# Optimization experiments

Measured on AMD Instinct MI355X. Metric: run time of the kernel, lower is better.

## Reference

```python
import jax, jax.numpy as jnp
import numpy as np

HEADS = 16

def _split_qkv(qkv, h):
    # faithful to rearrange 'b t (d k h) -> k b h t d' with k=3
    b, t, e3 = qkv.shape
    d = e3 // (3 * h)
    qkv = qkv.reshape(b, t, d, 3, h)          # (b,t,d,k,h), d-major packing
    qkv = jnp.transpose(qkv, (3, 0, 4, 1, 2))  # (k,b,h,t,d)
    return qkv[0], qkv[1], qkv[2]

def setup_inputs() -> dict:
    key = jax.random.key(0)
    ks = jax.random.split(key, 5)
    b, t, e = 2, 2048, 1024
    s = e ** -0.5
    return {
        "x": jax.random.normal(ks[0], (b, t, e), jnp.float32),
        "tx": jax.random.normal(ks[1], (b, t, e), jnp.float32),
        "Wqkv": jax.random.normal(ks[2], (3 * e, e), jnp.float32) * s,
        "Wtqkv": jax.random.normal(ks[3], (3 * e, e), jnp.float32) * s,
        "Wout": jax.random.normal(ks[4], (e, e), jnp.float32) * s,
    }

def reference(x, tx, Wqkv, Wtqkv, Wout):
    h = HEADS
    e = x.shape[-1]
    d_head = e // h
    scale = jnp.float32(d_head ** 0.5)  # NOTE: module MULTIPLIES by sqrt(d_head)

    qkv = x @ Wqkv.T     # (b,t,3e)
    tqkv = tx @ Wtqkv.T  # (b,t,3e)
    _q, k, v = _split_qkv(qkv, h)      # each (b,h,t,d)
    tq, _tk, _tv = _split_qkv(tqkv, h)

    energy = jnp.einsum('bhid,bhjd->bhij', tq, k) * scale  # (b,h,t,t)
    attn = jax.nn.softmax(energy, axis=-1)
    out = jnp.einsum('bhij,bhjd->bhid', attn, v)           # (b,h,t,d)
    b, _, t, d = out.shape
    out = jnp.transpose(out, (0, 2, 1, 3)).reshape(b, t, h * d)  # 'b h t d -> b t (h d)'
    return out @ Wout.T
```

## Files before the change

### kernel.cpp

```cpp
#include <hip/hip_runtime.h>

typedef unsigned short u16;
typedef unsigned int u32;
typedef __attribute__((ext_vector_type(8))) short short8;
typedef __attribute__((ext_vector_type(4))) float f32x4;

__device__ inline u16 f32_to_bf16(float f) {
  u32 u = __float_as_uint(f);
  u += 0x7fffu + ((u >> 16) & 1u);
  return (u16)(u >> 16);
}
__device__ inline float bf16_to_f32(u16 s) {
  return __uint_as_float(((u32)s) << 16);
}

#if __has_builtin(__builtin_amdgcn_exp2f)
#define EXP2F(x) __builtin_amdgcn_exp2f(x)
#else
#define EXP2F(x) exp2f(x)
#endif

__device__ inline void dma16(const void* gp, void* lp) {
  __builtin_amdgcn_global_load_lds(
      (const __attribute__((address_space(1))) u32*)gp,
      (__attribute__((address_space(3))) u32*)lp, 16, 0, 0);
}

__device__ inline u32 pack_hi16(u32 a, u32 b) {
  return __builtin_amdgcn_perm(b, a, 0x07060302u);
}
__device__ inline uint4 pack_bf16_8(const uint4 a, const uint4 b) {
  uint4 r;
  r.x = pack_hi16(a.x, a.y);
  r.y = pack_hi16(a.z, a.w);
  r.z = pack_hi16(b.x, b.y);
  r.w = pack_hi16(b.z, b.w);
  return r;
}
__device__ inline void split8(const uint4 a, const uint4 b, uint4& hi, uint4& lo) {
  u32 u[8] = {a.x, a.y, a.z, a.w, b.x, b.y, b.z, b.w};
  u32 l[8];
#pragma unroll
  for (int j = 0; j < 8; ++j)
    l[j] = __float_as_uint(__uint_as_float(u[j]) - __uint_as_float(u[j] & 0xffff0000u));
  hi.x = pack_hi16(u[0], u[1]); hi.y = pack_hi16(u[2], u[3]);
  hi.z = pack_hi16(u[4], u[5]); hi.w = pack_hi16(u[6], u[7]);
  lo.x = pack_hi16(l[0], l[1]); lo.y = pack_hi16(l[2], l[3]);
  lo.z = pack_hi16(l[4], l[5]); lo.w = pack_hi16(l[6], l[7]);
}

__global__ void repack_w(const float* __restrict__ Wqkv, const float* __restrict__ Wtqkv,
                         const float* __restrict__ Wout,
                         u16* __restrict__ Wtq_hi, u16* __restrict__ Wtq_lo,
                         u16* __restrict__ Wk_hi,  u16* __restrict__ Wk_lo,
                         u16* __restrict__ Wv_hi,  u16* __restrict__ Woutb) {
  int r = blockIdx.x;
  int part = r >> 10;
  int rr = r & 1023;
  int h = rr >> 6, d = rr & 63;
  const float* src;
  u16 *dh, *dl = nullptr;
  if (part == 0)      { src = Wtqkv + (size_t)(d * 48 + h) * 1024;      dh = Wtq_hi + (size_t)rr * 1024; dl = Wtq_lo + (size_t)rr * 1024; }
  else if (part == 1) { src = Wqkv  + (size_t)(d * 48 + 16 + h) * 1024; dh = Wk_hi  + (size_t)rr * 1024; dl = Wk_lo  + (size_t)rr * 1024; }
  else if (part == 2) { src = Wqkv  + (size_t)(d * 48 + 32 + h) * 1024; dh = Wv_hi  + (size_t)rr * 1024; }
  else                { src = Wout  + (size_t)rr * 1024;                dh = Woutb  + (size_t)rr * 1024; }
  int c = threadIdx.x * 4;
  f32x4 v = *(const f32x4*)&src[c];
  u32 hv[4], lv[4];
#pragma unroll
  for (int j = 0; j < 4; ++j) {
    u16 hb = f32_to_bf16(v[j]);
    hv[j] = hb;
    lv[j] = f32_to_bf16(v[j] - bf16_to_f32(hb));
  }
  uint2 ho; ho.x = hv[0] | (hv[1] << 16); ho.y = hv[2] | (hv[3] << 16);
  *(uint2*)&dh[c] = ho;
  if (dl) {
    uint2 lo; lo.x = lv[0] | (lv[1] << 16); lo.y = lv[2] | (lv[3] << 16);
    *(uint2*)&dl[c] = lo;
  }
}

__global__ __launch_bounds__(256) __attribute__((amdgpu_waves_per_eu(2)))
void proj_fused(const float* __restrict__ x, const float* __restrict__ tx,
                const u16* __restrict__ Wtq_hi, const u16* __restrict__ Wtq_lo,
                const u16* __restrict__ Wk_hi,  const u16* __restrict__ Wk_lo,
                const u16* __restrict__ Wv_hi,
                u16* __restrict__ Qhi, u16* __restrict__ Qlo,
                u16* __restrict__ Khi, u16* __restrict__ Klo,
                u16* __restrict__ Vt, float qscale) {
  __shared__ __align__(16) float Fs[2][128][32];
  __shared__ __align__(16) u16   Hs[2][128][32];
  __shared__ __align__(16) u16   Ls[2][128][32];
  const int tid = threadIdx.x;
  const int wid = tid >> 6, lane = tid & 63;
  const int g = lane >> 4, l16 = lane & 15;
  const int job = blockIdx.y;
  const int tile = blockIdx.x;
  const int wm = (wid & 1) * 64, wn = (wid >> 1) * 64;

  int m0, n0, N, frow0, hrow0;
  const float* Fsrc;
  const u16 *Hsrc;
  const u16 *Lsrc = nullptr;
  if (job == 0) {
    m0 = (tile >> 3) * 128; n0 = (tile & 7) * 128; N = 1024;
    Fsrc = tx; frow0 = m0; Hsrc = Wtq_hi; Lsrc = Wtq_lo; hrow0 = n0;
  } else if (job == 1) {
    m0 = (tile >> 3) * 128; n0 = (tile & 7) * 128; N = 1024;
    Fsrc = x; frow0 = m0; Hsrc = Wk_hi; Lsrc = Wk_lo; hrow0 = n0;
  } else {
    m0 = (tile >> 5) * 128; n0 = (tile & 31) * 128; N = 4096;
    Fsrc = x; frow0 = n0; Hsrc = Wv_hi; hrow0 = m0;
  }

  const int lrow8 = lane >> 3;
  const int gf = (lane & 7) ^ lrow8;
  const int lrow4 = lane >> 2;
  const int gh = (lane & 3) ^ ((lrow4 ^ (lrow4 >> 2)) & 3);

  auto issue_chunk = [&](int k0, int p) {
#pragma unroll
    for (int t = 0; t < 4; ++t) {
      int rb = wid * 32 + t * 8;
      dma16(&Fsrc[(size_t)(frow0 + rb + lrow8) * 1024 + k0 + gf * 4], &Fs[p][rb][0]);
    }
#pragma unroll
    for (int t = 0; t < 2; ++t) {
      int rb = wid * 32 + t * 16;
      size_t ro = (size_t)(hrow0 + rb + lrow4) * 1024 + k0 + gh * 8;
      dma16(&Hsrc[ro], &Hs[p][rb][0]);
      if (job != 2) dma16(&Lsrc[ro], &Ls[p][rb][0]);
    }
  };

  f32x4 acc[4][4];
  const f32x4 zero4 = {0.f, 0.f, 0.f, 0.f};
#pragma unroll
  for (int i = 0; i < 4; ++i)
#pragma unroll
    for (int j = 0; j < 4; ++j) acc[i][j] = zero4;

  const int sw8 = l16 & 7;
  const int sw4 = (l16 ^ (l16 >> 2)) & 3;

  issue_chunk(0, 0);

  for (int k0 = 0; k0 < 1024; k0 += 32) {
    const int p = (k0 >> 5) & 1;
    __syncthreads();
    if (k0 + 32 < 1024) issue_chunk(k0 + 32, p ^ 1);

    if (job != 2) {
      short8 ah[4], al[4], bh4[4], bl4[4];
#pragma unroll
      for (int mi = 0; mi < 4; ++mi) {
        const int R = wm + mi * 16 + l16;
        uint4 u0 = *(const uint4*)&Fs[p][R][((2 * g) ^ sw8) * 4];
        uint4 u1 = *(const uint4*)&Fs[p][R][((2 * g + 1) ^ sw8) * 4];
        uint4 hi, lo;
        split8(u0, u1, hi, lo);
        ah[mi] = *(short8*)&hi;
        al[mi] = *(short8*)&lo;
      }
#pragma unroll
      for (int ni = 0; ni < 4; ++ni) {
        const int R = wn + ni * 16 + l16;
        const int col = (g ^ sw4) * 8;
        bh4[ni] = *(const short8*)&Hs[p][R][col];
        bl4[ni] = *(const short8*)&Ls[p][R][col];
      }
#pragma unroll
      for (int mi = 0; mi < 4; ++mi)
#pragma unroll
        for (int ni = 0; ni < 4; ++ni) {
          acc[mi][ni] = __builtin_amdgcn_mfma_f32_16x16x32_bf16(ah[mi], bh4[ni], acc[mi][ni], 0, 0, 0);
          acc[mi][ni] = __builtin_amdgcn_mfma_f32_16x16x32_bf16(ah[mi], bl4[ni], acc[mi][ni], 0, 0, 0);
          acc[mi][ni] = __builtin_amdgcn_mfma_f32_16x16x32_bf16(al[mi], bh4[ni], acc[mi][ni], 0, 0, 0);
        }
    } else {
      short8 av[4], bx[4];
#pragma unroll
      for (int mi = 0; mi < 4; ++mi)
        av[mi] = *(const short8*)&Hs[p][wm + mi * 16 + l16][(g ^ sw4) * 8];
#pragma unroll
      for (int ni = 0; ni < 4; ++ni) {
        const int R = wn + ni * 16 + l16;
        uint4 u0 = *(const uint4*)&Fs[p][R][((2 * g) ^ sw8) * 4];
        uint4 u1 = *(const uint4*)&Fs[p][R][((2 * g + 1) ^ sw8) * 4];
        uint4 t = pack_bf16_8(u0, u1);
        bx[ni] = *(short8*)&t;
      }
#pragma unroll
      for (int mi = 0; mi < 4; ++mi)
#pragma unroll
        for (int ni = 0; ni < 4; ++ni)
          acc[mi][ni] = __builtin_amdgcn_mfma_f32_16x16x32_bf16(av[mi], bx[ni], acc[mi][ni], 0, 0, 0);
    }
  }

  u16* Chi = (job == 0) ? Qhi : ((job == 1) ? Khi : Vt);
  u16* Clo = (job == 0) ? Qlo : Klo;
  float scale = (job == 0) ? qscale : 1.0f;
#pragma unroll
  for (int mi = 0; mi < 4; ++mi)
#pragma unroll
    for (int ni = 0; ni < 4; ++ni) {
      int row = m0 + wm + mi * 16 + g * 4;
      int col = n0 + wn + ni * 16 + l16;
#pragma unroll
      for (int r = 0; r < 4; ++r) {
        float v = acc[mi][ni][r] * scale;
        size_t o = (size_t)(row + r) * N + col;
        u32 uv = __float_as_uint(v);
        if (job != 2) {
          Chi[o] = (u16)(uv >> 16);
          float lo = v - __uint_as_float(uv & 0xffff0000u);
          Clo[o] = (u16)(__float_as_uint(lo) >> 16);
        } else {
          Chi[o] = (u16)(uv >> 16);
        }
      }
    }
}

__global__ __launch_bounds__(256) __attribute__((amdgpu_waves_per_eu(2, 4)))
void gemm_out(const u16* __restrict__ A, const u16* __restrict__ B,
              float* __restrict__ C, int M, int N, int K) {
  __shared__ __align__(16) u16 As[128][40];
  __shared__ __align__(16) u16 Bs[64][40];
  const int tid = threadIdx.x;
  const int wid = tid >> 6, lane = tid & 63;
  const int g = lane >> 4, l16 = lane & 15;
  const int m0 = blockIdx.y * 128, n0 = blockIdx.x * 64;
  const int wm = (wid & 1) * 64, wn = (wid >> 1) * 32;

  f32x4 acc[4][2];
  const f32x4 zero4 = {0.f, 0.f, 0.f, 0.f};
#pragma unroll
  for (int i = 0; i < 4; ++i)
#pragma unroll
    for (int j = 0; j < 2; ++j) acc[i][j] = zero4;

  uint4 pa[2], pb;
  const int rowA0 = tid >> 2, colA = (tid & 3) * 8;
  const int rowA1 = rowA0 + 64;
  const int rowB = tid >> 2, colB = (tid & 3) * 8;
  pa[0] = *(const uint4*)&A[(size_t)(m0 + rowA0) * K + colA];
  pa[1] = *(const uint4*)&A[(size_t)(m0 + rowA1) * K + colA];
  pb    = *(const uint4*)&B[(size_t)(n0 + rowB) * K + colB];

  for (int k0 = 0; k0 < K; k0 += 32) {
    __syncthreads();
    *(uint4*)&As[rowA0][colA] = pa[0];
    *(uint4*)&As[rowA1][colA] = pa[1];
    *(uint4*)&Bs[rowB][colB] = pb;
    __syncthreads();
    if (k0 + 32 < K) {
      pa[0] = *(const uint4*)&A[(size_t)(m0 + rowA0) * K + k0 + 32 + colA];
      pa[1] = *(const uint4*)&A[(size_t)(m0 + rowA1) * K + k0 + 32 + colA];
      pb    = *(const uint4*)&B[(size_t)(n0 + rowB) * K + k0 + 32 + colB];
    }
    short8 af[4], bfr[2];
#pragma unroll
    for (int mi = 0; mi < 4; ++mi)
      af[mi] = *(const short8*)&As[wm + mi * 16 + l16][g * 8];
#pragma unroll
    for (int ni = 0; ni < 2; ++ni)
      bfr[ni] = *(const short8*)&Bs[wn + ni * 16 + l16][g * 8];
#pragma unroll
    for (int mi = 0; mi < 4; ++mi)
#pragma unroll
      for (int ni = 0; ni < 2; ++ni)
        acc[mi][ni] = __builtin_amdgcn_mfma_f32_16x16x32_bf16(af[mi], bfr[ni], acc[mi][ni], 0, 0, 0);
  }
#pragma unroll
  for (int mi = 0; mi < 4; ++mi)
#pragma unroll
    for (int ni = 0; ni < 2; ++ni) {
      int row = m0 + wm + mi * 16 + g * 4;
      int col = n0 + wn + ni * 16 + l16;
#pragma unroll
      for (int r = 0; r < 4; ++r)
        C[(size_t)(row + r) * N + col] = acc[mi][ni][r];
    }
}

__global__ __launch_bounds__(256)
void attn_fwd(const u16* __restrict__ Qhi, const u16* __restrict__ Qlo,
              const u16* __restrict__ Khi, const u16* __restrict__ Klo,
              const u16* __restrict__ Vt, u16* __restrict__ O) {
  const int blk = blockIdx.x;
  const int qb = blk & 15, bh = blk >> 4;
  const int h = bh & 15, b = bh >> 4;
  const int t0 = qb * 128;
  const int tid = threadIdx.x, wid = tid >> 6, lane = tid & 63;
  const int g = lane >> 4, l16 = lane & 15;

  __shared__ __align__(16) u16 Ksh[2][64][64];
  __shared__ __align__(16) u16 Ksl[2][64][64];
  __shared__ __align__(16) u16 Vs[2][64][64];
  __shared__ __align__(16) u16 Ps[4][32][72];

  const int lrow = lane >> 3;
  const int lgc  = (lane & 7) ^ lrow;
  const size_t kbase = (size_t)(b * 2048) * 1024 + h * 64;
  const size_t vbase = (size_t)(h * 64) * 4096 + b * 2048;

  auto issue_chunk = [&](int j0, int p) {
#pragma unroll
    for (int t = 0; t < 2; ++t) {
      int rbase = wid * 16 + t * 8;
      int row = rbase + lrow;
      dma16(&Khi[kbase + (size_t)(j0 + row) * 1024 + lgc * 8], &Ksh[p][rbase][0]);
      dma16(&Klo[kbase + (size_t)(j0 + row) * 1024 + lgc * 8], &Ksl[p][rbase][0]);
      dma16(&Vt[vbase + (size_t)row * 4096 + j0 + lgc * 8],    &Vs[p][rbase][0]);
    }
  };

  short8 qh[2][2], ql[2][2];
#pragma unroll
  for (int mt = 0; mt < 2; ++mt)
#pragma unroll
    for (int ks = 0; ks < 2; ++ks) {
      size_t qo = (size_t)(b * 2048 + t0 + wid * 32 + mt * 16 + l16) * 1024
                  + h * 64 + ks * 32 + g * 8;
      qh[mt][ks] = *(const short8*)&Qhi[qo];
      ql[mt][ks] = *(const short8*)&Qlo[qo];
    }

  float mrow[2][4];
#pragma unroll
  for (int mt = 0; mt < 2; ++mt)
#pragma unroll
    for (int r = 0; r < 4; ++r) mrow[mt][r] = -1.0e30f;
  const f32x4 zero4 = {0.f, 0.f, 0.f, 0.f};
  f32x4 acc[2][5];
#pragma unroll
  for (int mt = 0; mt < 2; ++mt)
#pragma unroll
    for (int dn = 0; dn < 5; ++dn) acc[mt][dn] = zero4;

  short8 ones8;
#pragma unroll
  for (int j = 0; j < 8; ++j) ones8[j] = (short)0x3f80;

  issue_chunk(0, 0);

  for (int i = 0; i < 32; ++i) {
    const int p = i & 1;
    __syncthreads();
    if (i < 31) issue_chunk((i + 1) * 64, 1 - p);

    f32x4 s[2][4];
#pragma unroll
    for (int mt = 0; mt < 2; ++mt)
#pragma unroll
      for (int n = 0; n < 4; ++n) s[mt][n] = zero4;
#pragma unroll
    for (int ks = 0; ks < 2; ++ks)
#pragma unroll
      for (int n = 0; n < 4; ++n) {
        int col = (((ks * 4 + g) ^ (l16 & 7))) * 8;
        short8 kh = *(const short8*)&Ksh[p][n * 16 + l16][col];
        short8 kl = *(const short8*)&Ksl[p][n * 16 + l16][col];
        s[0][n] = __builtin_amdgcn_mfma_f32_16x16x32_bf16(qh[0][ks], kh, s[0][n], 0, 0, 0);
        s[1][n] = __builtin_amdgcn_mfma_f32_16x16x32_bf16(qh[1][ks], kh, s[1][n], 0, 0, 0);
        s[0][n] = __builtin_amdgcn_mfma_f32_16x16x32_bf16(ql[0][ks], kh, s[0][n], 0, 0, 0);
        s[1][n] = __builtin_amdgcn_mfma_f32_16x16x32_bf16(ql[1][ks], kh, s[1][n], 0, 0, 0);
        s[0][n] = __builtin_amdgcn_mfma_f32_16x16x32_bf16(qh[0][ks], kl, s[0][n], 0, 0, 0);
        s[1][n] = __builtin_amdgcn_mfma_f32_16x16x32_bf16(qh[1][ks], kl, s[1][n], 0, 0, 0);
      }

#pragma unroll
    for (int mt = 0; mt < 2; ++mt)
#pragma unroll
      for (int r = 0; r < 4; ++r) {
        float cm = fmaxf(fmaxf(s[mt][0][r], s[mt][1][r]),
                         fmaxf(s[mt][2][r], s[mt][3][r]));
        cm = fmaxf(cm, __shfl_xor(cm, 1));
        cm = fmaxf(cm, __shfl_xor(cm, 2));
        cm = fmaxf(cm, __shfl_xor(cm, 4));
        cm = fmaxf(cm, __shfl_xor(cm, 8));
        float mnew = fmaxf(mrow[mt][r], cm);
        float al = EXP2F(mrow[mt][r] - mnew);
        mrow[mt][r] = mnew;
#pragma unroll
        for (int dn = 0; dn < 5; ++dn) acc[mt][dn][r] *= al;
        int qr = mt * 16 + g * 4 + r;
#pragma unroll
        for (int n = 0; n < 4; ++n) {
          float pv = EXP2F(s[mt][n][r] - mnew);
          Ps[wid][qr][n * 16 + l16] = (u16)(__float_as_uint(pv) >> 16);
        }
      }

#pragma unroll
    for (int ks2 = 0; ks2 < 2; ++ks2) {
      short8 pa0 = *(const short8*)&Ps[wid][l16][ks2 * 32 + g * 8];
      short8 pa1 = *(const short8*)&Ps[wid][16 + l16][ks2 * 32 + g * 8];
#pragma unroll
      for (int dn = 0; dn < 4; ++dn) {
        int col = (((ks2 * 4 + g) ^ (l16 & 7))) * 8;
        short8 vb = *(const short8*)&Vs[p][dn * 16 + l16][col];
        acc[0][dn] = __builtin_amdgcn_mfma_f32_16x16x32_bf16(pa0, vb, acc[0][dn], 0, 0, 0);
        acc[1][dn] = __builtin_amdgcn_mfma_f32_16x16x32_bf16(pa1, vb, acc[1][dn], 0, 0, 0);
      }
      acc[0][4] = __builtin_amdgcn_mfma_f32_16x16x32_bf16(pa0, ones8, acc[0][4], 0, 0, 0);
      acc[1][4] = __builtin_amdgcn_mfma_f32_16x16x32_bf16(pa1, ones8, acc[1][4], 0, 0, 0);
    }
  }

#pragma unroll
  for (int mt = 0; mt < 2; ++mt)
#pragma unroll
    for (int r = 0; r < 4; ++r) {
      float inv = 1.f / acc[mt][4][r];
      int row = t0 + wid * 32 + mt * 16 + g * 4 + r;
      size_t base = (size_t)(b * 2048 + row) * 1024 + h * 64;
#pragma unroll
      for (int dn = 0; dn < 4; ++dn)
        O[base + dn * 16 + l16] = (u16)(__float_as_uint(acc[mt][dn][r] * inv) >> 16);
    }
}

extern "C" void kernel_launch(void* const* d_in, const int* in_sizes, int n_in,
                              void* d_out, int out_size, void* d_ws, size_t ws_size,
                              hipStream_t stream) {
  const float* x     = (const float*)d_in[0];
  const float* tx    = (const float*)d_in[1];
  const float* Wqkv  = (const float*)d_in[2];
  const float* Wtqkv = (const float*)d_in[3];
  const float* Wout  = (const float*)d_in[4];
  float* out = (float*)d_out;

  char* ws = (char*)d_ws;
  const size_t MB = 1048576;
  u16* Wtq_hi = (u16*)(ws + 0 * MB);
  u16* Wtq_lo = (u16*)(ws + 2 * MB);
  u16* Wk_hi  = (u16*)(ws + 4 * MB);
  u16* Wk_lo  = (u16*)(ws + 6 * MB);
  u16* Wv_hi  = (u16*)(ws + 8 * MB);
  u16* Woutb  = (u16*)(ws + 10 * MB);
  u16* Qhi    = (u16*)(ws + 12 * MB);
  u16* Qlo    = (u16*)(ws + 20 * MB);
  u16* Khi    = (u16*)(ws + 28 * MB);
  u16* Klo    = (u16*)(ws + 36 * MB);
  u16* Vt     = (u16*)(ws + 44 * MB);
  u16* Ob     = (u16*)(ws + 0 * MB);
  if (ws_size < 52 * MB) return;

  const float QSCALE = 8.0f * 1.4426950408889634f;

  repack_w<<<4096, 256, 0, stream>>>(Wqkv, Wtqkv, Wout,
                                     Wtq_hi, Wtq_lo, Wk_hi, Wk_lo, Wv_hi, Woutb);
  proj_fused<<<dim3(256, 3), 256, 0, stream>>>(x, tx, Wtq_hi, Wtq_lo, Wk_hi, Wk_lo,
                                               Wv_hi, Qhi, Qlo, Khi, Klo, Vt, QSCALE);
  attn_fwd<<<512, 256, 0, stream>>>(Qhi, Qlo, Khi, Klo, Vt, Ob);
  gemm_out<<<dim3(16, 32), 256, 0, stream>>>(Ob, Woutb, out, 4096, 1024, 1024);
}
```

Baseline: 348.0 us.

## Transpose attention MFMAs to keep P in registers instead of LDS

Swaps the MFMA operand order so S and O are computed transposed, which puts each query row in a lane's column. The softmax max then reduces over the lane's own registers plus two cross-lane shuffles instead of four shuffles per element. P is packed to bf16 and redistributed with shuffles rather than round-tripping through the per-wave LDS buffer. The output is written with vectorized 8-byte stores. This removes LDS traffic and shared memory but adds shuffle and select work, and it relies on a pack_hi16 helper that must exist elsewhere in the file.

```diff
diff --git a/kernel.cpp b/kernel.cpp
--- a/kernel.cpp
+++ b/kernel.cpp
@@ -296,11 +296,12 @@
   const int t0 = qb * 128;
   const int tid = threadIdx.x, wid = tid >> 6, lane = tid & 63;
   const int g = lane >> 4, l16 = lane & 15;
+  const int par = g & 1;
+  const int hi2 = g >> 1;
 
   __shared__ __align__(16) u16 Ksh[2][64][64];
   __shared__ __align__(16) u16 Ksl[2][64][64];
   __shared__ __align__(16) u16 Vs[2][64][64];
-  __shared__ __align__(16) u16 Ps[4][32][72];
 
   const int lrow = lane >> 3;
   const int lgc  = (lane & 7) ^ lrow;
@@ -329,11 +330,7 @@
       ql[mt][ks] = *(const short8*)&Qlo[qo];
     }
 
-  float mrow[2][4];
-#pragma unroll
-  for (int mt = 0; mt < 2; ++mt)
-#pragma unroll
-    for (int r = 0; r < 4; ++r) mrow[mt][r] = -1.0e30f;
+  float mrow[2] = {-1.0e30f, -1.0e30f};
   const f32x4 zero4 = {0.f, 0.f, 0.f, 0.f};
   f32x4 acc[2][5];
 #pragma unroll
@@ -344,6 +341,8 @@
   short8 ones8;
 #pragma unroll
   for (int j = 0; j < 8; ++j) ones8[j] = (short)0x3f80;
+
+  union PB { u32 w[4]; short8 v; };
 
   issue_chunk(0, 0);
 
@@ -364,64 +363,82 @@
         int col = (((ks * 4 + g) ^ (l16 & 7))) * 8;
         short8 kh = *(const short8*)&Ksh[p][n * 16 + l16][col];
         short8 kl = *(const short8*)&Ksl[p][n * 16 + l16][col];
-        s[0][n] = __builtin_amdgcn_mfma_f32_16x16x32_bf16(qh[0][ks], kh, s[0][n], 0, 0, 0);
-        s[1][n] = __builtin_amdgcn_mfma_f32_16x16x32_bf16(qh[1][ks], kh, s[1][n], 0, 0, 0);
-        s[0][n] = __builtin_amdgcn_mfma_f32_16x16x32_bf16(ql[0][ks], kh, s[0][n], 0, 0, 0);
-        s[1][n] = __builtin_amdgcn_mfma_f32_16x16x32_bf16(ql[1][ks], kh, s[1][n], 0, 0, 0);
-        s[0][n] = __builtin_amdgcn_mfma_f32_16x16x32_bf16(qh[0][ks], kl, s[0][n], 0, 0, 0);
-        s[1][n] = __builtin_amdgcn_mfma_f32_16x16x32_bf16(qh[1][ks], kl, s[1][n], 0, 0, 0);
-      }
-
-#pragma unroll
-    for (int mt = 0; mt < 2; ++mt)
-#pragma unroll
-      for (int r = 0; r < 4; ++r) {
-        float cm = fmaxf(fmaxf(s[mt][0][r], s[mt][1][r]),
-                         fmaxf(s[mt][2][r], s[mt][3][r]));
-        cm = fmaxf(cm, __shfl_xor(cm, 1));
-        cm = fmaxf(cm, __shfl_xor(cm, 2));
-        cm = fmaxf(cm, __shfl_xor(cm, 4));
-        cm = fmaxf(cm, __shfl_xor(cm, 8));
-        float mnew = fmaxf(mrow[mt][r], cm);
-        float al = EXP2F(mrow[mt][r] - mnew);
-        mrow[mt][r] = mnew;
-#pragma unroll
-        for (int dn = 0; dn < 5; ++dn) acc[mt][dn][r] *= al;
-        int qr = mt * 16 + g * 4 + r;
-#pragma unroll
-        for (int n = 0; n < 4; ++n) {
-          float pv = EXP2F(s[mt][n][r] - mnew);
-          Ps[wid][qr][n * 16 + l16] = (u16)(__float_as_uint(pv) >> 16);
+        s[0][n] = __builtin_amdgcn_mfma_f32_16x16x32_bf16(kh, qh[0][ks], s[0][n], 0, 0, 0);
+        s[1][n] = __builtin_amdgcn_mfma_f32_16x16x32_bf16(kh, qh[1][ks], s[1][n], 0, 0, 0);
+        s[0][n] = __builtin_amdgcn_mfma_f32_16x16x32_bf16(kh, ql[0][ks], s[0][n], 0, 0, 0);
+        s[1][n] = __builtin_amdgcn_mfma_f32_16x16x32_bf16(kh, ql[1][ks], s[1][n], 0, 0, 0);
+        s[0][n] = __builtin_amdgcn_mfma_f32_16x16x32_bf16(kl, qh[0][ks], s[0][n], 0, 0, 0);
+        s[1][n] = __builtin_amdgcn_mfma_f32_16x16x32_bf16(kl, qh[1][ks], s[1][n], 0, 0, 0);
+      }
+
+    PB pb[2][2];
+#pragma unroll
+    for (int mt = 0; mt < 2; ++mt) {
+      float cm = -1.0e30f;
+#pragma unroll
+      for (int n = 0; n < 4; ++n)
+#pragma unroll
+        for (int r = 0; r < 4; ++r) cm = fmaxf(cm, s[mt][n][r]);
+      cm = fmaxf(cm, __shfl_xor(cm, 16));
+      cm = fmaxf(cm, __shfl_xor(cm, 32));
+      float mnew = fmaxf(mrow[mt], cm);
+      float al = EXP2F(mrow[mt] - mnew);
+      mrow[mt] = mnew;
+#pragma unroll
+      for (int dn = 0; dn < 5; ++dn)
+#pragma unroll
+        for (int r = 0; r < 4; ++r) acc[mt][dn][r] *= al;
+
+      u32 pk[4][2];
+#pragma unroll
+      for (int n = 0; n < 4; ++n) {
+        float p0 = EXP2F(s[mt][n][0] - mnew);
+        float p1 = EXP2F(s[mt][n][1] - mnew);
+        float p2 = EXP2F(s[mt][n][2] - mnew);
+        float p3 = EXP2F(s[mt][n][3] - mnew);
+        pk[n][0] = pack_hi16(__float_as_uint(p0), __float_as_uint(p1));
+        pk[n][1] = pack_hi16(__float_as_uint(p2), __float_as_uint(p3));
+      }
+#pragma unroll
+      for (int ks2 = 0; ks2 < 2; ++ks2)
+#pragma unroll
+        for (int t = 0; t < 4; ++t) {
+          int src = (((par << 1) | (t >> 1)) << 4) | l16;
+          u32 w0 = (u32)__shfl((int)pk[2 * ks2][t & 1], src);
+          u32 w1 = (u32)__shfl((int)pk[2 * ks2 + 1][t & 1], src);
+          pb[mt][ks2].w[t] = hi2 ? w1 : w0;
         }
-      }
+    }
 
 #pragma unroll
     for (int ks2 = 0; ks2 < 2; ++ks2) {
-      short8 pa0 = *(const short8*)&Ps[wid][l16][ks2 * 32 + g * 8];
-      short8 pa1 = *(const short8*)&Ps[wid][16 + l16][ks2 * 32 + g * 8];
 #pragma unroll
       for (int dn = 0; dn < 4; ++dn) {
         int col = (((ks2 * 4 + g) ^ (l16 & 7))) * 8;
         short8 vb = *(const short8*)&Vs[p][dn * 16 + l16][col];
-        acc[0][dn] = __builtin_amdgcn_mfma_f32_16x16x32_bf16(pa0, vb, acc[0][dn], 0, 0, 0);
-        acc[1][dn] = __builtin_amdgcn_mfma_f32_16x16x32_bf16(pa1, vb, acc[1][dn], 0, 0, 0);
-      }
-      acc[0][4] = __builtin_amdgcn_mfma_f32_16x16x32_bf16(pa0, ones8, acc[0][4], 0, 0, 0);
-      acc[1][4] = __builtin_amdgcn_mfma_f32_16x16x32_bf16(pa1, ones8, acc[1][4], 0, 0, 0);
-    }
-  }
-
-#pragma unroll
-  for (int mt = 0; mt < 2; ++mt)
-#pragma unroll
-    for (int r = 0; r < 4; ++r) {
-      float inv = 1.f / acc[mt][4][r];
-      int row = t0 + wid * 32 + mt * 16 + g * 4 + r;
-      size_t base = (size_t)(b * 2048 + row) * 1024 + h * 64;
-#pragma unroll
-      for (int dn = 0; dn < 4; ++dn)
-        O[base + dn * 16 + l16] = (u16)(__float_as_uint(acc[mt][dn][r] * inv) >> 16);
-    }
+        acc[0][dn] = __builtin_amdgcn_mfma_f32_16x16x32_bf16(vb, pb[0][ks2].v, acc[0][dn], 0, 0, 0);
+        acc[1][dn] = __builtin_amdgcn_mfma_f32_16x16x32_bf16(vb, pb[1][ks2].v, acc[1][dn], 0, 0, 0);
+      }
+      acc[0][4] = __builtin_amdgcn_mfma_f32_16x16x32_bf16(ones8, pb[0][ks2].v, acc[0][4], 0, 0, 0);
+      acc[1][4] = __builtin_amdgcn_mfma_f32_16x16x32_bf16(ones8, pb[1][ks2].v, acc[1][4], 0, 0, 0);
+    }
+  }
+
+#pragma unroll
+  for (int mt = 0; mt < 2; ++mt) {
+    float inv = 1.f / acc[mt][4][0];
+    int qrow = t0 + wid * 32 + mt * 16 + l16;
+    size_t base = (size_t)(b * 2048 + qrow) * 1024 + h * 64;
+#pragma unroll
+    for (int dn = 0; dn < 4; ++dn) {
+      u32 o0 = pack_hi16(__float_as_uint(acc[mt][dn][0] * inv),
+                         __float_as_uint(acc[mt][dn][1] * inv));
+      u32 o1 = pack_hi16(__float_as_uint(acc[mt][dn][2] * inv),
+                         __float_as_uint(acc[mt][dn][3] * inv));
+      uint2 ov; ov.x = o0; ov.y = o1;
+      *(uint2*)&O[base + dn * 16 + g * 4] = ov;
+    }
+  }
 }
 
 extern "C" void kernel_launch(void* const* d_in, const int* in_sizes, int n_in,
```

Result: faster. 316.8 us (-9.0%).
